# Optimization experiments

Hardware: AMD Instinct MI355X
Metric: run time of the kernel (lower is better)

Reference implementation:

```python
import jax, jax.numpy as jnp
import numpy as np

B, T, DFEAT = 2, 2048, 1024
DIM, DEPTH, H, DH = 512, 2, 8, 64
INNER = H * DH  # 512
MLP = 512
RED1, RED2 = DIM // 16, DIM // 32  # 32, 16
EPS = 1e-5


def _ln(x, g, b):
    m = jnp.mean(x, axis=-1, keepdims=True)
    v = jnp.mean((x - m) ** 2, axis=-1, keepdims=True)
    return (x - m) * jax.lax.rsqrt(v + EPS) * g + b


def _bn_eval(x, g, b, rm, rv):
    # x: [B, C, T]; eval-mode BatchNorm1d with running stats
    return (x - rm[:, None]) * jax.lax.rsqrt(rv[:, None] + EPS) * g[:, None] + b[:, None]


def setup_inputs() -> dict:
    key = jax.random.key(0)
    ks = iter(jax.random.split(key, 64))
    rn = lambda shape, s=0.02: (jax.random.normal(next(ks), shape, dtype=jnp.float32) * s)
    inp = {}
    inp['x'] = jax.random.normal(next(ks), (B, T, DFEAT), dtype=jnp.float32)
    # Temporal embedding conv (k=3, pad=1), OIW layout
    inp['emb_w'] = rn((DIM, DFEAT, 3))
    inp['emb_b'] = jnp.zeros((DIM,), jnp.float32)
    # Transformer: stacked per-layer params [DEPTH, ...]
    inp['ln1_g'] = jnp.ones((DEPTH, DIM), jnp.float32)
    inp['ln1_b'] = jnp.zeros((DEPTH, DIM), jnp.float32)
    inp['wqkvt'] = rn((DEPTH, DIM, 4 * INNER))
    inp['wout'] = rn((DEPTH, 2 * INNER, DIM))
    inp['bout'] = jnp.zeros((DEPTH, DIM), jnp.float32)
    inp['ln2_g'] = jnp.ones((DEPTH, DIM), jnp.float32)
    inp['ln2_b'] = jnp.zeros((DEPTH, DIM), jnp.float32)
    inp['w1'] = rn((DEPTH, DIM, MLP))
    inp['b1'] = jnp.zeros((DEPTH, MLP), jnp.float32)
    inp['w2'] = rn((DEPTH, MLP, DIM))
    inp['b2'] = jnp.zeros((DEPTH, DIM), jnp.float32)
    # NormalHead (k=1 convs -> pointwise), eval-mode BN params
    inp['h1_w'] = rn((RED1, DIM)); inp['h1_b'] = jnp.zeros((RED1,), jnp.float32)
    inp['bn1_g'] = jnp.ones((RED1,), jnp.float32); inp['bn1_b'] = jnp.zeros((RED1,), jnp.float32)
    inp['bn1_m'] = jnp.zeros((RED1,), jnp.float32); inp['bn1_v'] = jnp.ones((RED1,), jnp.float32)
    inp['h2_w'] = rn((RED2, RED1)); inp['h2_b'] = jnp.zeros((RED2,), jnp.float32)
    inp['bn2_g'] = jnp.ones((RED2,), jnp.float32); inp['bn2_b'] = jnp.zeros((RED2,), jnp.float32)
    inp['bn2_m'] = jnp.zeros((RED2,), jnp.float32); inp['bn2_v'] = jnp.ones((RED2,), jnp.float32)
    inp['h3_w'] = rn((1, RED2)); inp['h3_b'] = jnp.zeros((1,), jnp.float32)
    return inp


def _attention(x, wqkvt, wout, bout, attn2):
    b, n, d = x.shape
    qkvt = x @ wqkvt  # [b, n, 4*INNER]
    q, k, v, t = jnp.split(qkvt, 4, axis=-1)
    sp = lambda z: z.reshape(b, n, H, DH).transpose(0, 2, 1, 3)  # b h n d
    q, k, v, t = sp(q), sp(k), sp(v), sp(t)
    scale = DH ** -0.5
    dots = jnp.einsum('bhid,bhjd->bhij', q, k) * scale
    attn1 = jax.nn.softmax(dots, axis=-1)
    out1 = jnp.einsum('bhij,bhjd->bhid', attn1, v)
    out2 = jnp.einsum('ij,bhjd->bhid', attn2, t)
    out = jnp.concatenate([out1, out2], axis=-1)  # b h n 2*DH
    out = out.transpose(0, 2, 1, 3).reshape(b, n, 2 * INNER)
    return out @ wout + bout


def _forward(x, emb_w, emb_b, ln1_g, ln1_b, wqkvt, wout, bout, ln2_g, ln2_b,
             w1, b1, w2, b2, h1_w, h1_b, bn1_g, bn1_b, bn1_m, bn1_v,
             h2_w, h2_b, bn2_g, bn2_b, bn2_m, bn2_v, h3_w, h3_b):
    # Temporal embedding: Conv1d(k=3,pad=1) + ReLU over time axis
    xc = x.transpose(0, 2, 1)  # [B, DFEAT, T]
    emb = jax.lax.conv_general_dilated(xc, emb_w, (1,), 'SAME',
                                       dimension_numbers=('NCH', 'OIH', 'NCH'))
    emb = jax.nn.relu(emb + emb_b[None, :, None])
    h = emb.transpose(0, 2, 1)  # [B, T, DIM]
    # fixed temporal-decay attention matrix (batch/head independent)
    idx = jnp.arange(T, dtype=jnp.float32)
    tg = jnp.abs(idx[None, :] - idx[:, None])
    a2 = jnp.exp(-tg / jnp.float32(np.e))
    attn2 = a2 / a2.sum(-1)  # torch broadcast: divide along last axis
    for l in range(DEPTH):
        h = h + _attention(_ln(h, ln1_g[l], ln1_b[l]), wqkvt[l], wout[l], bout[l], attn2)
        z = _ln(h, ln2_g[l], ln2_b[l])
        z = jax.nn.gelu(z @ w1[l] + b1[l], approximate=False) @ w2[l] + b2[l]
        h = h + z
    # NormalHead on [B, DIM, T] with k=1 convs
    y = h.transpose(0, 2, 1)
    f1 = jnp.einsum('oc,bct->bot', h1_w, y) + h1_b[None, :, None]
    f2 = jnp.einsum('oc,bct->bot', h2_w, jax.nn.relu(_bn_eval(f1, bn1_g, bn1_b, bn1_m, bn1_v))) + h2_b[None, :, None]
    f3 = jnp.einsum('oc,bct->bot', h3_w, jax.nn.relu(_bn_eval(f2, bn2_g, bn2_b, bn2_m, bn2_v))) + h3_b[None, :, None]
    scores = jax.nn.sigmoid(f3)[:, 0, :]  # [B, T]
    return scores


def reference(x, emb_w, emb_b, ln1_g, ln1_b, wqkvt, wout, bout, ln2_g, ln2_b,
              w1, b1, w2, b2, h1_w, h1_b, bn1_g, bn1_b, bn1_m, bn1_v,
              h2_w, h2_b, bn2_g, bn2_b, bn2_m, bn2_v, h3_w, h3_b):
    return _forward(x, emb_w, emb_b, ln1_g, ln1_b, wqkvt, wout, bout, ln2_g, ln2_b,
                    w1, b1, w2, b2, h1_w, h1_b, bn1_g, bn1_b, bn1_m, bn1_v,
                    h2_w, h2_b, bn2_g, bn2_b, bn2_m, bn2_v, h3_w, h3_b)
```

## Files before the change

### kernel.cpp

```cpp
#include <hip/hip_runtime.h>
#include <hip/hip_bf16.h>
#include <math.h>

#define TN 2048
#define BN 2
#define DF 1024
#define DM 512
#define NHD 8
#define DHD 64
#define INV_E 0.36787944117144233f

typedef float f32x4 __attribute__((ext_vector_type(4)));
typedef __bf16 bf16x8 __attribute__((ext_vector_type(8)));
typedef unsigned short ushort8 __attribute__((ext_vector_type(8)));
typedef unsigned short ushort4v __attribute__((ext_vector_type(4)));
typedef unsigned short u16;

__device__ inline u16 f2bf(float f) {
    __hip_bfloat16 b = __float2bfloat16(f);
    return __builtin_bit_cast(u16, b);
}
__device__ inline float bf2f(u16 u) {
    unsigned int x = ((unsigned int)u) << 16;
    return __builtin_bit_cast(float, x);
}
__device__ inline bf16x8 ldbf8(const u16* p) {
    return __builtin_bit_cast(bf16x8, *(const ushort8*)p);
}

struct WtrAll {
    const float* src[8];
    u16* dst[8];
    int K[8], N[8], start[8], mask[8], shift[8];
};

__global__ __launch_bounds__(256) void wtr_all_kernel(WtrAll a) {
    __shared__ u16 tile[64][67];
    int bid = blockIdx.x;
    int w = 0;
#pragma unroll
    for (int i = 1; i < 8; ++i)
        if (bid >= a.start[i]) w = i;
    const float* src = a.src[w];
    u16* dst = a.dst[w];
    int K = a.K[w], N = a.N[w];
    int t0 = bid - a.start[w];
    int bx = t0 & a.mask[w], by = t0 >> a.shift[w];
    int t = threadIdx.x;
    int tr = t >> 4, tc = (t & 15) * 4;
#pragma unroll
    for (int rr = 0; rr < 4; ++rr) {
        int kl = tr + rr * 16;
        float4 v = *(const float4*)&src[(size_t)(by * 64 + kl) * N + bx * 64 + tc];
        tile[kl][tc + 0] = f2bf(v.x);
        tile[kl][tc + 1] = f2bf(v.y);
        tile[kl][tc + 2] = f2bf(v.z);
        tile[kl][tc + 3] = f2bf(v.w);
    }
    __syncthreads();
#pragma unroll
    for (int rr = 0; rr < 4; ++rr) {
        int nl = tr + rr * 16;
        ushort4v o;
#pragma unroll
        for (int q = 0; q < 4; ++q) o[q] = tile[tc + q][nl];
        *(ushort4v*)&dst[(size_t)(bx * 64 + nl) * K + by * 64 + tc] = o;
    }
}

__global__ __launch_bounds__(256) void emb_tr_kernel(const float* __restrict__ w,
                                                     u16* __restrict__ dst) {
    int idx = blockIdx.x * 256 + threadIdx.x;
    if (idx >= DM * 3 * DF) return;
    int o = idx / (3 * DF);
    int rem = idx - o * 3 * DF;
    int tap = rem / DF, i = rem - tap * DF;
    dst[idx] = f2bf(w[(size_t)o * 3 * DF + i * 3 + tap]);
}

__global__ __launch_bounds__(256) void sinv_kernel(float* __restrict__ sinv) {
    int j = blockIdx.x * 256 + threadIdx.x;
    if (j >= TN) return;
    float r = __expf(-INV_E);
    float inv1mr = 1.f / (1.f - r);
    float a = (1.f - __expf(-(float)(j + 1) * INV_E)) * inv1mr;
    float b = (r - __expf(-(float)(TN - j) * INV_E)) * inv1mr;
    sinv[j] = 1.f / (a + b);
}

__global__ __launch_bounds__(256) void xshift_kernel(const float* __restrict__ x,
                                                     u16* __restrict__ xs) {
    int idx = blockIdx.x * 256 + threadIdx.x;
    if (idx >= BN * TN * 3 * DF / 8) return;
    int row = idx / (3 * DF / 8);
    int kc = (idx - row * (3 * DF / 8)) * 8;
    int b = row >> 11, t = row & (TN - 1);
    int tap = kc / DF, i = kc - tap * DF;
    int tt = t + tap - 1;
    ushort8 o;
    if (tt < 0 || tt >= TN) {
        for (int q = 0; q < 8; ++q) o[q] = 0;
    } else {
        const float4* p = (const float4*)&x[((size_t)b * TN + tt) * DF + i];
        float4 v0 = p[0], v1 = p[1];
        o[0] = f2bf(v0.x); o[1] = f2bf(v0.y); o[2] = f2bf(v0.z); o[3] = f2bf(v0.w);
        o[4] = f2bf(v1.x); o[5] = f2bf(v1.y); o[6] = f2bf(v1.z); o[7] = f2bf(v1.w);
    }
    *(ushort8*)&xs[(size_t)row * 3 * DF + kc] = o;
}

template <int MODE, int BM, int BNT>
__global__ __launch_bounds__(256) void gemm2(const u16* __restrict__ A,
                                             const u16* __restrict__ Bt,
                                             const float* __restrict__ bias,
                                             const float* resid, void* outp,
                                             int M, int N, int K) {
    constexpr int MR = BM / 32, NR = BNT / 32;
    constexpr int PA = BM / 64, PB = BNT / 64;
    __shared__ __align__(16) u16 As[2][BM][72];
    __shared__ __align__(16) u16 Bs[2][BNT][72];
    int tid = threadIdx.x;
    int lane = tid & 63, wid = tid >> 6;
    int m0 = blockIdx.y * BM, n0 = blockIdx.x * BNT;
    int wm = (wid >> 1) * (BM / 2), wn = (wid & 1) * (BNT / 2);
    int fr = lane & 15, kq = (lane >> 4) * 8;
    int srow = tid >> 2, scol = (tid & 3) * 16;
    f32x4 acc[MR][NR] = {};
    const u16* Ap = A + (size_t)(m0 + srow) * K + scol;
    const u16* Bp = Bt + (size_t)(n0 + srow) * K + scol;
    ushort8 ra[PA][2], rb[PB][2];
#pragma unroll
    for (int p = 0; p < PA; ++p) {
        ra[p][0] = *(const ushort8*)(Ap + (size_t)p * 64 * K);
        ra[p][1] = *(const ushort8*)(Ap + (size_t)p * 64 * K + 8);
    }
#pragma unroll
    for (int p = 0; p < PB; ++p) {
        rb[p][0] = *(const ushort8*)(Bp + (size_t)p * 64 * K);
        rb[p][1] = *(const ushort8*)(Bp + (size_t)p * 64 * K + 8);
    }
    int nt = K >> 6;
    int pb = 0;
    for (int t = 0; t < nt; ++t) {
#pragma unroll
        for (int p = 0; p < PA; ++p) {
            *(ushort8*)&As[pb][srow + p * 64][scol] = ra[p][0];
            *(ushort8*)&As[pb][srow + p * 64][scol + 8] = ra[p][1];
        }
#pragma unroll
        for (int p = 0; p < PB; ++p) {
            *(ushort8*)&Bs[pb][srow + p * 64][scol] = rb[p][0];
            *(ushort8*)&Bs[pb][srow + p * 64][scol + 8] = rb[p][1];
        }
        __syncthreads();
        if (t + 1 < nt) {
            int ko = (t + 1) << 6;
#pragma unroll
            for (int p = 0; p < PA; ++p) {
                ra[p][0] = *(const ushort8*)(Ap + (size_t)p * 64 * K + ko);
                ra[p][1] = *(const ushort8*)(Ap + (size_t)p * 64 * K + ko + 8);
            }
#pragma unroll
            for (int p = 0; p < PB; ++p) {
                rb[p][0] = *(const ushort8*)(Bp + (size_t)p * 64 * K + ko);
                rb[p][1] = *(const ushort8*)(Bp + (size_t)p * 64 * K + ko + 8);
            }
        }
#pragma unroll
        for (int kc = 0; kc < 2; ++kc) {
            bf16x8 af[MR], bf[NR];
#pragma unroll
            for (int a = 0; a < MR; ++a) af[a] = ldbf8(&As[pb][wm + a * 16 + fr][kc * 32 + kq]);
#pragma unroll
            for (int b = 0; b < NR; ++b) bf[b] = ldbf8(&Bs[pb][wn + b * 16 + fr][kc * 32 + kq]);
#pragma unroll
            for (int a = 0; a < MR; ++a)
#pragma unroll
                for (int b = 0; b < NR; ++b)
                    acc[a][b] = __builtin_amdgcn_mfma_f32_16x16x32_bf16(af[a], bf[b], acc[a][b], 0, 0, 0);
        }
        pb ^= 1;
    }
    int rq = (lane >> 4) * 4;
#pragma unroll
    for (int a = 0; a < MR; ++a)
#pragma unroll
        for (int b = 0; b < NR; ++b) {
            int col = n0 + wn + b * 16 + fr;
            float bv = (MODE & 1) ? bias[col] : 0.f;
#pragma unroll
            for (int r = 0; r < 4; ++r) {
                int row = m0 + wm + a * 16 + rq + r;
                float v = acc[a][b][r] + bv;
                if (MODE & 2) v = fmaxf(v, 0.f);
                if (MODE & 4) v = 0.5f * v * (1.f + erff(v * 0.7071067811865476f));
                if (MODE & 8) v += resid[(size_t)row * N + col];
                if (MODE & 16) ((float*)outp)[(size_t)row * N + col] = v;
                else           ((u16*)outp)[(size_t)row * N + col] = f2bf(v);
            }
        }
}

__global__ __launch_bounds__(256) void ln_kernel(const float* __restrict__ h,
                                                 const float* __restrict__ g,
                                                 const float* __restrict__ bta,
                                                 u16* __restrict__ outp) {
    int lane = threadIdx.x & 63, wid = threadIdx.x >> 6;
    int row = blockIdx.x * 4 + wid;
    const float4* xp = (const float4*)(h + (size_t)row * DM + lane * 8);
    float4 v0 = xp[0], v1 = xp[1];
    float v[8] = {v0.x, v0.y, v0.z, v0.w, v1.x, v1.y, v1.z, v1.w};
    float s = 0.f;
#pragma unroll
    for (int i = 0; i < 8; ++i) s += v[i];
    for (int sft = 1; sft < 64; sft <<= 1) s += __shfl_xor(s, sft, 64);
    float mean = s * (1.f / DM);
    float q = 0.f;
#pragma unroll
    for (int i = 0; i < 8; ++i) { float d = v[i] - mean; q += d * d; }
    for (int sft = 1; sft < 64; sft <<= 1) q += __shfl_xor(q, sft, 64);
    float rs = rsqrtf(q * (1.f / DM) + 1e-5f);
    ushort8 o;
#pragma unroll
    for (int i = 0; i < 8; ++i) {
        float y = (v[i] - mean) * rs * g[lane * 8 + i] + bta[lane * 8 + i];
        o[i] = f2bf(y);
    }
    *(ushort8*)&outp[(size_t)row * DM + lane * 8] = o;
}

__global__ __launch_bounds__(256) void attn_split(const u16* __restrict__ qkvt,
                                                  u16* __restrict__ po,
                                                  float* __restrict__ pl) {
    __shared__ __align__(16) u16 Ks[64][72];
    __shared__ __align__(16) u16 Vs[64][72];
    __shared__ __align__(16) u16 Ps[4][16][72];
    int tid = threadIdx.x;
    int lane = tid & 63, wid = tid >> 6;
    int bid = blockIdx.x;
    int cc = bid & 3, qb = (bid >> 2) & 31, hh = (bid >> 7) & 7, b = bid >> 10;
    int fr = lane & 15, kq = (lane >> 4) * 8, rq = (lane >> 4) * 4;

    int qrow = qb * 64 + wid * 16 + fr;
    bf16x8 aq[2];
#pragma unroll
    for (int kc = 0; kc < 2; ++kc) {
        bf16x8 t = ldbf8(&qkvt[((size_t)(b * TN + qrow)) * 2048 + hh * 64 + kc * 32 + kq]);
        bf16x8 sc;
#pragma unroll
        for (int i = 0; i < 8; ++i) sc[i] = (__bf16)(0.125f * (float)t[i]);
        aq[kc] = sc;
    }

    f32x4 o[4];
#pragma unroll
    for (int cb = 0; cb < 4; ++cb) o[cb] = f32x4{0.f, 0.f, 0.f, 0.f};
    float rsum[4] = {0.f, 0.f, 0.f, 0.f};

    int srow = tid >> 3, scol = (tid & 7) * 8;
    int vxw = ((scol >> 3) & 7) << 3;
    int pxw = rq << 1;
    for (int kb = 0; kb < 8; ++kb) {
        int j0 = cc * 512 + kb * 64;
#pragma unroll
        for (int half = 0; half < 2; ++half) {
            int jr = srow + half * 32;
            size_t rbase = ((size_t)(b * TN + j0 + jr)) * 2048;
            *(ushort8*)&Ks[jr][scol] = *(const ushort8*)&qkvt[rbase + 512 + hh * 64 + scol];
            ushort8 vv = *(const ushort8*)&qkvt[rbase + 1024 + hh * 64 + scol];
            int jc = jr ^ vxw;
#pragma unroll
            for (int i = 0; i < 8; ++i) Vs[scol + i][jc] = vv[i];
        }
        __syncthreads();
#pragma unroll
        for (int jb = 0; jb < 4; ++jb) {
            f32x4 sa = f32x4{0.f, 0.f, 0.f, 0.f};
#pragma unroll
            for (int kc = 0; kc < 2; ++kc) {
                bf16x8 bk = ldbf8(&Ks[jb * 16 + fr][kc * 32 + kq]);
                sa = __builtin_amdgcn_mfma_f32_16x16x32_bf16(aq[kc], bk, sa, 0, 0, 0);
            }
#pragma unroll
            for (int r = 0; r < 4; ++r) {
                float p = __expf(sa[r]);
                rsum[r] += p;
                Ps[wid][rq + r][(jb * 16 + fr) ^ pxw] = f2bf(p);
            }
        }
        bf16x8 pa[2];
#pragma unroll
        for (int kc = 0; kc < 2; ++kc)
            pa[kc] = ldbf8(&Ps[wid][fr][(kc * 32 + kq) ^ ((fr & 12) << 1)]);
#pragma unroll
        for (int cb = 0; cb < 4; ++cb)
#pragma unroll
            for (int kc = 0; kc < 2; ++kc) {
                int vrow = cb * 16 + fr;
                bf16x8 bv = ldbf8(&Vs[vrow][(kc * 32 + kq) ^ (((vrow >> 3) & 7) << 3)]);
                o[cb] = __builtin_amdgcn_mfma_f32_16x16x32_bf16(pa[kc], bv, o[cb], 0, 0, 0);
            }
        __syncthreads();
    }
#pragma unroll
    for (int r = 0; r < 4; ++r)
        for (int sft = 1; sft < 16; sft <<= 1) rsum[r] += __shfl_xor(rsum[r], sft, 64);
#pragma unroll
    for (int r = 0; r < 4; ++r) {
        int grow = (b * NHD + hh) * TN + qb * 64 + wid * 16 + rq + r;
        size_t pidx = (size_t)grow * 4 + cc;
#pragma unroll
        for (int cb = 0; cb < 4; ++cb)
            po[pidx * 64 + cb * 16 + fr] = f2bf(o[cb][r]);
        if (fr == 0) pl[pidx] = rsum[r];
    }
}

__global__ __launch_bounds__(256) void attn_combine(const u16* __restrict__ po,
                                                    const float* __restrict__ pl,
                                                    u16* __restrict__ attcat) {
    int lane = threadIdx.x & 63, wid = threadIdx.x >> 6;
    int R = blockIdx.x * 4 + wid;
    float l = 0.f, ov = 0.f;
#pragma unroll
    for (int cc = 0; cc < 4; ++cc) {
        l += pl[R * 4 + cc];
        ov += bf2f(po[((size_t)R * 4 + cc) * 64 + lane]);
    }
    int bh = R >> 11, q = R & (TN - 1);
    int b = bh >> 3, hh = bh & 7;
    attcat[((size_t)(b * TN + q)) * 1024 + hh * 128 + lane] = f2bf(ov / l);
}

__global__ __launch_bounds__(512) void band_kernel(const u16* __restrict__ qkvt,
                                                   const float* __restrict__ sinv,
                                                   u16* __restrict__ attcat) {
    __shared__ float pw[33];
    int tid = threadIdx.x;
    if (tid < 33) pw[tid] = __expf(-(float)tid * INV_E);
    __syncthreads();
    int i = blockIdx.x & (TN - 1), b = blockIdx.x >> 11;
    int c = tid;
    int j0 = i - 32; if (j0 < 0) j0 = 0;
    int j1 = i + 32; if (j1 > TN - 1) j1 = TN - 1;
    float acc = 0.f;
    for (int j = j0; j <= j1; ++j) {
        int m = i - j; if (m < 0) m = -m;
        float w = pw[m] * sinv[j];
        acc = fmaf(w, bf2f(qkvt[((size_t)(b * TN + j)) * 2048 + 1536 + c]), acc);
    }
    int outcol = (c >> 6) * 128 + 64 + (c & 63);
    attcat[((size_t)(b * TN + i)) * 1024 + outcol] = f2bf(acc);
}

__global__ __launch_bounds__(256) void head_kernel(
    const float* __restrict__ h, const float* __restrict__ h1w, const float* __restrict__ h1b,
    const float* __restrict__ bn1g, const float* __restrict__ bn1b,
    const float* __restrict__ bn1m, const float* __restrict__ bn1v,
    const float* __restrict__ h2w, const float* __restrict__ h2b,
    const float* __restrict__ bn2g, const float* __restrict__ bn2b,
    const float* __restrict__ bn2m, const float* __restrict__ bn2v,
    const float* __restrict__ h3w, const float* __restrict__ h3b,
    float* __restrict__ outp) {
    int lane = threadIdx.x & 63, wid = threadIdx.x >> 6;
    int idx = blockIdx.x * 4 + wid;
    const float4* xp = (const float4*)(h + (size_t)idx * DM + lane * 8);
    float4 v0 = xp[0], v1 = xp[1];
    float v[8] = {v0.x, v0.y, v0.z, v0.w, v1.x, v1.y, v1.z, v1.w};
    float a1[32];
#pragma unroll
    for (int o = 0; o < 32; ++o) {
        const float4* wp = (const float4*)(h1w + (size_t)o * DM + lane * 8);
        float4 w0 = wp[0], w1v = wp[1];
        a1[o] = w0.x * v[0] + w0.y * v[1] + w0.z * v[2] + w0.w * v[3] +
                w1v.x * v[4] + w1v.y * v[5] + w1v.z * v[6] + w1v.w * v[7];
    }
    for (int sft = 1; sft < 64; sft <<= 1) {
#pragma unroll
        for (int o = 0; o < 32; ++o) a1[o] += __shfl_xor(a1[o], sft, 64);
    }
    float r1[32];
#pragma unroll
    for (int o = 0; o < 32; ++o) {
        float f = a1[o] + h1b[o];
        f = (f - bn1m[o]) * rsqrtf(bn1v[o] + 1e-5f) * bn1g[o] + bn1b[o];
        r1[o] = fmaxf(f, 0.f);
    }
    float r2[16];
#pragma unroll
    for (int p = 0; p < 16; ++p) {
        float s = h2b[p];
#pragma unroll
        for (int o = 0; o < 32; ++o) s = fmaf(h2w[p * 32 + o], r1[o], s);
        s = (s - bn2m[p]) * rsqrtf(bn2v[p] + 1e-5f) * bn2g[p] + bn2b[p];
        r2[p] = fmaxf(s, 0.f);
    }
    float f3 = h3b[0];
#pragma unroll
    for (int p = 0; p < 16; ++p) f3 = fmaf(h3w[p], r2[p], f3);
    if (lane == 0) outp[idx] = 1.f / (1.f + __expf(-f3));
}

extern "C" void kernel_launch(void* const* d_in, const int* in_sizes, int n_in,
                              void* d_out, int out_size, void* d_ws, size_t ws_size,
                              hipStream_t stream) {
    const float* x     = (const float*)d_in[0];
    const float* emb_w = (const float*)d_in[1];
    const float* emb_b = (const float*)d_in[2];
    const float* ln1_g = (const float*)d_in[3];
    const float* ln1_b = (const float*)d_in[4];
    const float* wqkvt = (const float*)d_in[5];
    const float* wout  = (const float*)d_in[6];
    const float* bout  = (const float*)d_in[7];
    const float* ln2_g = (const float*)d_in[8];
    const float* ln2_b = (const float*)d_in[9];
    const float* w1    = (const float*)d_in[10];
    const float* b1    = (const float*)d_in[11];
    const float* w2    = (const float*)d_in[12];
    const float* b2    = (const float*)d_in[13];
    const float* h1w   = (const float*)d_in[14];
    const float* h1b   = (const float*)d_in[15];
    const float* bn1g  = (const float*)d_in[16];
    const float* bn1b  = (const float*)d_in[17];
    const float* bn1m  = (const float*)d_in[18];
    const float* bn1v  = (const float*)d_in[19];
    const float* h2w   = (const float*)d_in[20];
    const float* h2b   = (const float*)d_in[21];
    const float* bn2g  = (const float*)d_in[22];
    const float* bn2b  = (const float*)d_in[23];
    const float* bn2m  = (const float*)d_in[24];
    const float* bn2v  = (const float*)d_in[25];
    const float* h3w   = (const float*)d_in[26];
    const float* h3b   = (const float*)d_in[27];
    float* outp = (float*)d_out;

    char* ws = (char*)d_ws;
    size_t off = 0;
    auto take = [&](size_t bytes) {
        char* p = ws + off;
        off = (off + bytes + 255) & ~(size_t)255;
        return p;
    };
    const size_t MB = 1024 * 1024;
    float* h    = (float*)take((size_t)BN * TN * DM * 4);
    char* Pr    = take(18 * MB);
    u16* attcat = (u16*)take((size_t)BN * TN * 1024 * 2);
    float* sinv = (float*)take(TN * 4);
    u16* embwt  = (u16*)take((size_t)DM * 3 * DF * 2);
    u16* wqt    = (u16*)take((size_t)2 * 2048 * DM * 2);
    u16* woutt  = (u16*)take((size_t)2 * DM * 1024 * 2);
    u16* w1t    = (u16*)take((size_t)2 * DM * DM * 2);
    u16* w2t    = (u16*)take((size_t)2 * DM * DM * 2);
    u16* U      = (u16*)take((size_t)BN * TN * 3 * DF * 2);
    u16* xs = U;
    u16* qkvtb = U;
    u16* xln  = (u16*)Pr;
    u16* z1   = (u16*)(Pr + 4 * MB);
    float* pl = (float*)Pr;
    u16* po   = (u16*)(Pr + 1 * MB);
    (void)ws_size; (void)in_sizes; (void)n_in; (void)out_size;

    emb_tr_kernel<<<dim3(DM * 3 * DF / 256), dim3(256), 0, stream>>>(emb_w, embwt);
    {
        WtrAll a;
        int cur = 0;
        for (int l = 0; l < 2; ++l) {
            int e = l * 4;
            a.src[e + 0] = wqkvt + (size_t)l * 512 * 2048; a.dst[e + 0] = wqt + (size_t)l * 2048 * 512;
            a.K[e + 0] = 512;  a.N[e + 0] = 2048; a.start[e + 0] = cur; a.mask[e + 0] = 31; a.shift[e + 0] = 5; cur += 256;
            a.src[e + 1] = wout + (size_t)l * 1024 * 512;  a.dst[e + 1] = woutt + (size_t)l * 512 * 1024;
            a.K[e + 1] = 1024; a.N[e + 1] = 512;  a.start[e + 1] = cur; a.mask[e + 1] = 7;  a.shift[e + 1] = 3; cur += 128;
            a.src[e + 2] = w1 + (size_t)l * 512 * 512;     a.dst[e + 2] = w1t + (size_t)l * 512 * 512;
            a.K[e + 2] = 512;  a.N[e + 2] = 512;  a.start[e + 2] = cur; a.mask[e + 2] = 7;  a.shift[e + 2] = 3; cur += 64;
            a.src[e + 3] = w2 + (size_t)l * 512 * 512;     a.dst[e + 3] = w2t + (size_t)l * 512 * 512;
            a.K[e + 3] = 512;  a.N[e + 3] = 512;  a.start[e + 3] = cur; a.mask[e + 3] = 7;  a.shift[e + 3] = 3; cur += 64;
        }
        wtr_all_kernel<<<dim3(cur), dim3(256), 0, stream>>>(a);
    }
    sinv_kernel<<<dim3(TN / 256), dim3(256), 0, stream>>>(sinv);
    xshift_kernel<<<dim3(BN * TN * 3 * DF / 8 / 256), dim3(256), 0, stream>>>(x, xs);

    gemm2<19, 64, 64><<<dim3(DM / 64, BN * TN / 64), dim3(256), 0, stream>>>(
        xs, embwt, emb_b, nullptr, h, BN * TN, DM, 3 * DF);

    for (int l = 0; l < 2; ++l) {
        ln_kernel<<<dim3(BN * TN / 4), dim3(256), 0, stream>>>(h, ln1_g + l * DM, ln1_b + l * DM, xln);
        gemm2<0, 128, 128><<<dim3(2048 / 128, BN * TN / 128), dim3(256), 0, stream>>>(
            xln, wqt + (size_t)l * 2048 * 512, nullptr, nullptr, qkvtb, BN * TN, 2048, DM);
        attn_split<<<dim3(BN * NHD * (TN / 64) * 4), dim3(256), 0, stream>>>(qkvtb, po, pl);
        attn_combine<<<dim3(BN * NHD * TN / 4), dim3(256), 0, stream>>>(po, pl, attcat);
        band_kernel<<<dim3(BN * TN), dim3(512), 0, stream>>>(qkvtb, sinv, attcat);
        gemm2<25, 64, 64><<<dim3(DM / 64, BN * TN / 64), dim3(256), 0, stream>>>(
            attcat, woutt + (size_t)l * 512 * 1024, bout + l * DM, h, h, BN * TN, DM, 1024);
        ln_kernel<<<dim3(BN * TN / 4), dim3(256), 0, stream>>>(h, ln2_g + l * DM, ln2_b + l * DM, xln);
        gemm2<5, 64, 64><<<dim3(DM / 64, BN * TN / 64), dim3(256), 0, stream>>>(
            xln, w1t + (size_t)l * 512 * 512, b1 + l * DM, nullptr, z1, BN * TN, DM, DM);
        gemm2<25, 64, 64><<<dim3(DM / 64, BN * TN / 64), dim3(256), 0, stream>>>(
            z1, w2t + (size_t)l * 512 * 512, b2 + l * DM, h, h, BN * TN, DM, DM);
    }
    head_kernel<<<dim3(BN * TN / 4), dim3(256), 0, stream>>>(
        h, h1w, h1b, bn1g, bn1b, bn1m, bn1v, h2w, h2b, bn2g, bn2b, bn2m, bn2v, h3w, h3b, outp);
}
```

Before: 398.8 us.

## Replace windowed band convolution with chunked bidirectional exponential-decay scan

The banded temporal-attention term, a sum over a ±32 window weighted by exp(-|i-j|/e), is now computed as a forward and a backward first-order recurrence with decay r. Each thread handles 32 consecutive positions of one channel and warms up over 32 neighbouring positions on each side. This cuts per-output loads from about 65 to about 4. In exchange the window is no longer cut off sharply: positions inside a chunk pick up extra terms from more than 32 steps away, weighted by r^33 or smaller, so the result is a close approximation rather than exact.

```diff
diff --git a/kernel.cpp b/kernel.cpp
--- a/kernel.cpp
+++ b/kernel.cpp
@@ -9,6 +9,7 @@
 #define NHD 8
 #define DHD 64
 #define INV_E 0.36787944117144233f
+#define R_DECAY 0.69220062755534635f
 
 typedef float f32x4 __attribute__((ext_vector_type(4)));
 typedef __bf16 bf16x8 __attribute__((ext_vector_type(8)));
@@ -332,25 +333,43 @@
     attcat[((size_t)(b * TN + q)) * 1024 + hh * 128 + lane] = f2bf(ov / l);
 }
 
-__global__ __launch_bounds__(512) void band_kernel(const u16* __restrict__ qkvt,
-                                                   const float* __restrict__ sinv,
-                                                   u16* __restrict__ attcat) {
-    __shared__ float pw[33];
-    int tid = threadIdx.x;
-    if (tid < 33) pw[tid] = __expf(-(float)tid * INV_E);
-    __syncthreads();
-    int i = blockIdx.x & (TN - 1), b = blockIdx.x >> 11;
-    int c = tid;
-    int j0 = i - 32; if (j0 < 0) j0 = 0;
-    int j1 = i + 32; if (j1 > TN - 1) j1 = TN - 1;
-    float acc = 0.f;
-    for (int j = j0; j <= j1; ++j) {
-        int m = i - j; if (m < 0) m = -m;
-        float w = pw[m] * sinv[j];
-        acc = fmaf(w, bf2f(qkvt[((size_t)(b * TN + j)) * 2048 + 1536 + c]), acc);
+#define BCH 32
+__global__ __launch_bounds__(256) void band_scan_kernel(const u16* __restrict__ qkvt,
+                                                        const float* __restrict__ sinv,
+                                                        u16* __restrict__ attcat) {
+    int tid = blockIdx.x * 256 + threadIdx.x;
+    int c = tid & 511;
+    int rest = tid >> 9;
+    int chunk = rest & 63;
+    int b = rest >> 6;
+    int i0 = chunk * BCH;
+    const float r = R_DECAY;
+    const u16* tcol = qkvt + 1536 + c;
+    float regs[BCH];
+    float st = 0.f;
+    for (int j = i0 - 32; j < i0; ++j) {
+        if (j >= 0) st = r * st + sinv[j] * bf2f(tcol[(size_t)(b * TN + j) * 2048]);
+    }
+#pragma unroll
+    for (int k = 0; k < BCH; ++k) {
+        int j = i0 + k;
+        st = r * st + sinv[j] * bf2f(tcol[(size_t)(b * TN + j) * 2048]);
+        regs[k] = st;
+    }
+    st = 0.f;
+    for (int j = i0 + BCH + 31; j >= i0 + BCH; --j) {
+        if (j < TN) st = r * st + sinv[j] * bf2f(tcol[(size_t)(b * TN + j) * 2048]);
+    }
+#pragma unroll
+    for (int k = BCH - 1; k >= 0; --k) {
+        int j = i0 + k;
+        regs[k] += r * st;
+        st = r * st + sinv[j] * bf2f(tcol[(size_t)(b * TN + j) * 2048]);
     }
     int outcol = (c >> 6) * 128 + 64 + (c & 63);
-    attcat[((size_t)(b * TN + i)) * 1024 + outcol] = f2bf(acc);
+#pragma unroll
+    for (int k = 0; k < BCH; ++k)
+        attcat[((size_t)(b * TN + i0 + k)) * 1024 + outcol] = f2bf(regs[k]);
 }
 
 __global__ __launch_bounds__(256) void head_kernel(
@@ -489,7 +508,7 @@
             xln, wqt + (size_t)l * 2048 * 512, nullptr, nullptr, qkvtb, BN * TN, 2048, DM);
         attn_split<<<dim3(BN * NHD * (TN / 64) * 4), dim3(256), 0, stream>>>(qkvtb, po, pl);
         attn_combine<<<dim3(BN * NHD * TN / 4), dim3(256), 0, stream>>>(po, pl, attcat);
-        band_kernel<<<dim3(BN * TN), dim3(512), 0, stream>>>(qkvtb, sinv, attcat);
+        band_scan_kernel<<<dim3(BN * 512 * (TN / BCH) / 256), dim3(256), 0, stream>>>(qkvtb, sinv, attcat);
         gemm2<25, 64, 64><<<dim3(DM / 64, BN * TN / 64), dim3(256), 0, stream>>>(
             attcat, woutt + (size_t)l * 512 * 1024, bout + l * DM, h, h, BN * TN, DM, 1024);
         ln_kernel<<<dim3(BN * TN / 4), dim3(256), 0, stream>>>(h, ln2_g + l * DM, ln2_b + l * DM, xln);
```

After: 341.1 us. -14.5%, faster.
